# Optimization experiments

Measured on AMD Instinct MI355X. Metric: run time of the kernel, lower is better.

Reference implementation:

```python
import jax, jax.numpy as jnp
import numpy as np

B, S, H, NH, DH, F, L = 4, 2048, 512, 8, 64, 2048, 4
ALPHA = 1.0   # config.lag_time_scale_alpha
EPS = 1e-12   # BERT layer_norm_eps
MS_PER_MIN = 60.0 * 1000.0


def setup_inputs() -> dict:
    key = jax.random.key(0)
    ks = jax.random.split(key, 24)
    p = lambda k, shape: (jax.random.normal(k, shape, jnp.float32) * 0.02)
    inp = {
        "query_states": jax.random.normal(ks[0], (B, S, H), jnp.float32),
        "attention_mask": jnp.zeros((B, 1, 1, S), jnp.float32),
        "position_bias": jax.random.normal(ks[1], (1, NH, S, S), jnp.float32) * 0.02,
        "timestamp": jnp.sort(jax.random.randint(ks[2], (B, S), 0, 36_000_000, jnp.int32), axis=-1),
        # stacked per-layer parameters (L leading dim)
        "wq": p(ks[3], (L, H, H)), "bq": jnp.zeros((L, H), jnp.float32),
        "wk": p(ks[4], (L, H, H)), "bk": jnp.zeros((L, H), jnp.float32),
        "wv": p(ks[5], (L, H, H)), "bv": jnp.zeros((L, H), jnp.float32),
        "wo": p(ks[6], (L, H, H)), "bo": jnp.zeros((L, H), jnp.float32),
        "ln1_g": jnp.ones((L, H), jnp.float32), "ln1_b": jnp.zeros((L, H), jnp.float32),
        "wi": p(ks[7], (L, H, F)), "bi": jnp.zeros((L, F), jnp.float32),
        "wo2": p(ks[8], (L, F, H)), "bo2": jnp.zeros((L, H), jnp.float32),
        "ln2_g": jnp.ones((L, H), jnp.float32), "ln2_b": jnp.zeros((L, H), jnp.float32),
    }
    return inp


def _ln(x, g, b):
    m = x.mean(-1, keepdims=True)
    v = ((x - m) ** 2).mean(-1, keepdims=True)
    return (x - m) / jnp.sqrt(v + EPS) * g + b


def reference(query_states, attention_mask, position_bias, timestamp,
              wq, bq, wk, bk, wv, bv, wo, bo, ln1_g, ln1_b,
              wi, bi, wo2, bo2, ln2_g, ln2_b):
    # encoder (is_decoder=False) lag-time scale: (B,1,S,S)
    lag = (timestamp[:, None, :, None] - timestamp[:, None, None, :]).astype(jnp.float32) / MS_PER_MIN
    scale = np.sqrt(DH).astype(np.float32) - ALPHA / (jnp.clip(lag, 0.0) + 1.0) + ALPHA

    x = query_states
    for l in range(L):
        def proj(w, b):
            return (x @ w + b).reshape(B, S, NH, DH).transpose(0, 2, 1, 3)  # (B,NH,S,DH)
        q, k, v = proj(wq[l], bq[l]), proj(wk[l], bk[l]), proj(wv[l], bv[l])
        scores = jnp.einsum('bhqd,bhkd->bhqk', q, k) / scale + position_bias + attention_mask
        probs = jax.nn.softmax(scores, axis=-1)
        ctx = jnp.einsum('bhqk,bhkd->bhqd', probs, v).transpose(0, 2, 1, 3).reshape(B, S, H)
        attn = _ln(ctx @ wo[l] + bo[l] + x, ln1_g[l], ln1_b[l])
        ffn = jax.nn.gelu(attn @ wi[l] + bi[l], approximate=False) @ wo2[l] + bo2[l]
        x = _ln(ffn + attn, ln2_g[l], ln2_b[l])
    return x
```

## Files before the change

### kernel.cpp

```cpp
#include <hip/hip_runtime.h>
#include <stdint.h>

typedef unsigned short u16;
using half8   = __attribute__((ext_vector_type(8))) _Float16;
using half4v  = __attribute__((ext_vector_type(4))) _Float16;
using half2v  = __attribute__((ext_vector_type(2))) _Float16;
using float4v = __attribute__((ext_vector_type(4))) float;

#define L2E 1.4426950408889634f

__device__ inline float4v f4zero() { float4v z = {0.f, 0.f, 0.f, 0.f}; return z; }

__device__ inline u16 f2h(float f) {
  union { _Float16 h; u16 u; } v; v.h = (_Float16)f; return v.u;
}
__device__ inline float h2f(u16 u) {
  union { u16 u; _Float16 h; } v; v.u = u; return (float)v.h;
}

__device__ inline half2v cvtpk(float a, float b) {
  return __builtin_bit_cast(half2v, __builtin_amdgcn_cvt_pkrtz(a, b));
}
__device__ inline _Float16 hexp2_(_Float16 x) {
  _Float16 r;
  asm("v_exp_f16 %0, %1" : "=v"(r) : "v"(x));
  return r;
}
__device__ inline float fdot2f(half2v a, float c) {
#if __has_builtin(__builtin_amdgcn_fdot2)
  typedef __attribute__((ext_vector_type(2))) __fp16 h2r;
  return __builtin_amdgcn_fdot2(__builtin_bit_cast(h2r, a),
                                __builtin_bit_cast(h2r, 0x3C003C00u), c, false);
#else
  return c + (float)a.x + (float)a.y;
#endif
}

__device__ inline void glds16(const u16* g, u16* lds_base, int lane) {
#if __has_builtin(__builtin_amdgcn_global_load_lds)
  (void)lane;
  __builtin_amdgcn_global_load_lds((const __attribute__((address_space(1))) void*)g,
                                   (__attribute__((address_space(3))) void*)lds_base,
                                   16, 0, 0);
#else
  *(uint4*)(lds_base + (size_t)lane * 8) = *(const uint4*)g;
#endif
}

__global__ __launch_bounds__(256) void transpose_cast_kernel(
    const float* __restrict__ in, u16* __restrict__ out, int K, int N, size_t out_ls) {
  __shared__ float tile[32][33];
  const int tx = threadIdx.x & 31, ty = threadIdx.x >> 5;
  in  += (size_t)blockIdx.z * K * N;
  out += (size_t)blockIdx.z * out_ls;
  const int n  = blockIdx.x * 32 + tx;
  const int k0 = blockIdx.y * 32;
#pragma unroll
  for (int j = 0; j < 32; j += 8)
    tile[ty + j][tx] = in[(size_t)(k0 + ty + j) * N + n];
  __syncthreads();
  const int k = k0 + tx;
  const int n0 = blockIdx.x * 32;
#pragma unroll
  for (int j = 0; j < 32; j += 8)
    out[(size_t)(n0 + ty + j) * K + k] = f2h(tile[tx][ty + j]);
}

__global__ __launch_bounds__(256) void cast_kernel(const float* __restrict__ in,
                                                   u16* __restrict__ out) {
  const int i = (blockIdx.x * 256 + threadIdx.x) * 4;
  float4 t = *(const float4*)(in + i);
  ushort4 o;
  o.x = f2h(t.x); o.y = f2h(t.y); o.z = f2h(t.z); o.w = f2h(t.w);
  *(ushort4*)(out + i) = o;
}

__global__ __launch_bounds__(256) void pb_tile_kernel(const float* __restrict__ pb,
                                                      u16* __restrict__ pbT) {
  const int g  = blockIdx.x * 256 + threadIdx.x;
  const int mm = g & 15;
  const int q  = (g >> 4) & 2047;
  const int kbh = g >> 15;
  const int kb = kbh & 31, h = kbh >> 5;
  const float* src = pb + ((size_t)h * 2048 + q) * 2048 + kb * 64 + mm;
  ushort4 o;
  o.x = f2h(src[0]  * L2E);
  o.y = f2h(src[16] * L2E);
  o.z = f2h(src[32] * L2E);
  o.w = f2h(src[48] * L2E);
  *(ushort4*)(pbT + ((size_t)(h * 32 + kb) * 2048 + q) * 64 + mm * 4) = o;
}

__global__ __launch_bounds__(256) void inv_tile_kernel(const int* __restrict__ ts,
                                                       u16* __restrict__ invT) {
  const int g  = blockIdx.x * 256 + threadIdx.x;
  const int mm = g & 15;
  const int q  = (g >> 4) & 2047;
  const int kb = (g >> 15) & 31;
  const int b  = g >> 20;
  const int tq = ts[b * 2048 + q];
  ushort4 o;
  u16* op = (u16*)&o;
#pragma unroll
  for (int nb = 0; nb < 4; nb++) {
    const int k = kb * 64 + nb * 16 + mm;
    const int du = tq - ts[b * 2048 + k];
    const float u = (du > 0) ? (float)du : 0.f;
    op[nb] = f2h(fmaf(u, L2E, 86561.70245333781f) *
                 __builtin_amdgcn_rcpf(fmaf(u, 9.f, 480000.f)));
  }
  *(ushort4*)(invT + ((size_t)(b * 32 + kb) * 2048 + q) * 64 + mm * 4) = o;
}

__global__ __launch_bounds__(256) void maskts_kernel(const float* __restrict__ mask,
                                                     const int* __restrict__ ts,
                                                     float* __restrict__ maskE,
                                                     float* __restrict__ tsf) {
  const int i = blockIdx.x * 256 + threadIdx.x;
  maskE[i] = mask[i] * L2E;
  tsf[i]   = (float)ts[i];
}

template <int BM, int BN, int NN, int KK, int EPI>
__global__ __launch_bounds__(256) void gemm_kernel(
    const u16* __restrict__ A, const u16* __restrict__ Wt,
    const float* __restrict__ b0, const float* __restrict__ b1, const float* __restrict__ b2,
    const u16* __restrict__ resid,
    void* __restrict__ o0, void* __restrict__ o1, void* __restrict__ o2) {
  constexpr int FI = BM / 32;
  constexpr int FJB = BN / 32;
  constexpr int FIW = BM / 32;
  constexpr int FJW = BN / 32;
  __shared__ __align__(16) u16 As[BM * 64];
  __shared__ __align__(16) u16 Bs[BN * 64];
  const int tid = threadIdx.x, lane = tid & 63, wv = tid >> 6;
  const int quad = lane >> 4, mm = lane & 15;
  const int m0 = blockIdx.x * BM, n0 = blockIdx.y * BN;
  const int wm = (wv >> 1) * (BM / 2), wn = (wv & 1) * (BN / 2);
  const int srow = tid >> 3, slot = tid & 7;
  const int chunk = slot ^ (srow & 7);
  const u16* Ag = A  + (size_t)(m0 + srow) * KK + chunk * 8;
  const u16* Bg = Wt + (size_t)(n0 + srow) * KK + chunk * 8;
  u16* AsW = As + (size_t)(wv * 8) * 64;
  u16* BsW = Bs + (size_t)(wv * 8) * 64;
  const int sw = mm & 7;

  float4v acc[FIW][FJW];
#pragma unroll
  for (int i = 0; i < FIW; i++)
#pragma unroll
    for (int j = 0; j < FJW; j++) acc[i][j] = f4zero();

  for (int kt = 0; kt < KK; kt += 64) {
#pragma unroll
    for (int i = 0; i < FI; i++)
      glds16(Ag + (size_t)i * 32 * KK + kt, AsW + i * 32 * 64, lane);
#pragma unroll
    for (int j = 0; j < FJB; j++)
      glds16(Bg + (size_t)j * 32 * KK + kt, BsW + j * 32 * 64, lane);
    __syncthreads();
#pragma unroll
    for (int ks = 0; ks < 2; ks++) {
      half8 a[FIW], b[FJW];
#pragma unroll
      for (int i = 0; i < FIW; i++)
        a[i] = *(const half8*)(As + (size_t)(wm + i * 16 + mm) * 64 + (size_t)((ks * 4 + quad) ^ sw) * 8);
#pragma unroll
      for (int j = 0; j < FJW; j++)
        b[j] = *(const half8*)(Bs + (size_t)(wn + j * 16 + mm) * 64 + (size_t)((ks * 4 + quad) ^ sw) * 8);
#pragma unroll
      for (int i = 0; i < FIW; i++)
#pragma unroll
        for (int j = 0; j < FJW; j++)
          acc[i][j] = __builtin_amdgcn_mfma_f32_16x16x32_f16(a[i], b[j], acc[i][j], 0, 0, 0);
    }
    __syncthreads();
  }

#pragma unroll
  for (int j = 0; j < FJW; j++) {
    const int gn = n0 + wn + j * 16 + mm;
    if (EPI == 4) {
      const int which = gn >> 9, col = gn & 511, h = (gn >> 6) & 7, d = gn & 63;
      const float* bp = (which == 0) ? b0 : (which == 1) ? b1 : b2;
      const float bias = bp[col];
      u16* dst = (which == 0) ? (u16*)o0 : (which == 1) ? (u16*)o1 : (u16*)o2;
#pragma unroll
      for (int i = 0; i < FIW; i++)
#pragma unroll
        for (int r = 0; r < 4; r++) {
          const int gm = m0 + wm + i * 16 + quad * 4 + r;
          const int b_ = gm >> 11, s_ = gm & 2047;
          const float val = acc[i][j][r] + bias;
          if (which < 2)
            dst[((size_t)((b_ * 8 + h) * 2048 + s_)) * 64 + d] = f2h(val);
          else
            dst[((size_t)((b_ * 8 + h) * 64 + d)) * 2048 +
                (s_ & ~63) + (((s_ & 15) << 2) | ((s_ >> 4) & 3))] = f2h(val);
        }
    } else {
      const float bias = b0[gn];
#pragma unroll
      for (int i = 0; i < FIW; i++)
#pragma unroll
        for (int r = 0; r < 4; r++) {
          const int gm = m0 + wm + i * 16 + quad * 4 + r;
          const float val = acc[i][j][r] + bias;
          const size_t idx = (size_t)gm * NN + gn;
          if (EPI == 2) {
            ((float*)o0)[idx] = val + h2f(resid[idx]);
          } else {
            const float z  = val * 0.70710678118654752f;
            const float az = fabsf(z);
            const float t  = __builtin_amdgcn_rcpf(1.0f + 0.3275911f * az);
            const float poly = t * (0.254829592f + t * (-0.284496736f +
                               t * (1.421413741f + t * (-1.453152027f + t * 1.061405429f))));
            const float e = __builtin_amdgcn_exp2f(-az * az * L2E);
            float erf_ = 1.0f - poly * e;
            erf_ = (z < 0.0f) ? -erf_ : erf_;
            ((u16*)o0)[idx] = f2h(val * 0.5f * (1.0f + erf_));
          }
        }
    }
  }
}

template <int TILED>
__global__ __launch_bounds__(512) void flash4_kernel(
    const u16* __restrict__ Q, const u16* __restrict__ Kb, const u16* __restrict__ Vt,
    const u16* __restrict__ pbT, const u16* __restrict__ invT,
    const float* __restrict__ pb32,
    const float* __restrict__ maskE, const float* __restrict__ tsf,
    u16* __restrict__ ctx) {
  __shared__ __align__(16) u16 Kls[2][64 * 64];
  __shared__ __align__(16) u16 Vls[2][64 * 64];
  __shared__ __align__(16) u16 P[8][16 * 64];
  const int tid = threadIdx.x, lane = tid & 63, w = tid >> 6;
  const int quad = lane >> 4, mm = lane & 15;
  const int bh = blockIdx.y, b_ = bh >> 3, h_ = bh & 7;
  const int q0 = blockIdx.x * 128 + w * 16;
  const size_t qk_base = (size_t)bh * 2048 * 64;
  const size_t v_base  = (size_t)bh * 64 * 2048;
  const int srow = lane >> 3, slot = lane & 7;
  const int chunk = slot ^ srow;
  const int sw = mm & 7;

  const u16* Kgl = Kb + qk_base + (size_t)(w * 8 + srow) * 64 + chunk * 8;
  const u16* Vgl = Vt + v_base + (size_t)(w * 8 + srow) * 2048 + chunk * 8;

  glds16(Kgl, &Kls[0][(w * 8) * 64], lane);
  glds16(Vgl, &Vls[0][(w * 8) * 64], lane);

  half8 aq[2];
#pragma unroll
  for (int t = 0; t < 2; t++)
    aq[t] = *(const half8*)(Q + qk_base + (size_t)(q0 + mm) * 64 + t * 32 + quad * 8);

  float tqf[4];
  if (TILED < 2) {
#pragma unroll
    for (int r = 0; r < 4; r++) tqf[r] = tsf[b_ * 2048 + q0 + quad * 4 + r];
  }

  float l_r[4] = {0.f, 0.f, 0.f, 0.f};
  float4v o[4];
#pragma unroll
  for (int ob = 0; ob < 4; ob++) o[ob] = f4zero();

  ushort4 pbc[4], invc[4]; float tkc[4], mkc[4];
  if (TILED >= 1) {
#pragma unroll
    for (int r = 0; r < 4; r++)
      pbc[r] = *(const ushort4*)(pbT + ((size_t)(h_ * 32) * 2048 + q0 + quad * 4 + r) * 64 + mm * 4);
  }
  if (TILED == 2) {
#pragma unroll
    for (int r = 0; r < 4; r++)
      invc[r] = *(const ushort4*)(invT + ((size_t)(b_ * 32) * 2048 + q0 + quad * 4 + r) * 64 + mm * 4);
  } else {
#pragma unroll
    for (int nb = 0; nb < 4; nb++) tkc[nb] = tsf[b_ * 2048 + nb * 16 + mm];
  }
#pragma unroll
  for (int nb = 0; nb < 4; nb++) mkc[nb] = maskE[b_ * 2048 + nb * 16 + mm];

  int cur = 0;
  for (int kt = 0; kt < 32; kt++) {
    const int k0 = kt * 64;
    __syncthreads();

    const int kn = (kt < 31) ? kt + 1 : kt;
    ushort4 pbn[4], invn[4]; float tkn[4], mkn[4];
    if (TILED >= 1) {
#pragma unroll
      for (int r = 0; r < 4; r++)
        pbn[r] = *(const ushort4*)(pbT + ((size_t)(h_ * 32 + kn) * 2048 + q0 + quad * 4 + r) * 64 + mm * 4);
    }
    if (TILED == 2) {
#pragma unroll
      for (int r = 0; r < 4; r++)
        invn[r] = *(const ushort4*)(invT + ((size_t)(b_ * 32 + kn) * 2048 + q0 + quad * 4 + r) * 64 + mm * 4);
    } else {
#pragma unroll
      for (int nb = 0; nb < 4; nb++) tkn[nb] = tsf[b_ * 2048 + kn * 64 + nb * 16 + mm];
    }
#pragma unroll
    for (int nb = 0; nb < 4; nb++) mkn[nb] = maskE[b_ * 2048 + kn * 64 + nb * 16 + mm];

    if (kt < 31) {
      const size_t ko = (size_t)(kt + 1) * 4096;
      const size_t vo = (size_t)(kt + 1) * 64;
      glds16(Kgl + ko, &Kls[cur ^ 1][(w * 8) * 64], lane);
      glds16(Vgl + vo, &Vls[cur ^ 1][(w * 8) * 64], lane);
    }

    const u16* Kc = Kls[cur];
    float4v s[4];
    __builtin_amdgcn_s_setprio(1);
#pragma unroll
    for (int nb = 0; nb < 4; nb++) {
      const half8 kf0 = *(const half8*)(Kc + (size_t)(nb * 16 + mm) * 64 + (size_t)(quad ^ sw) * 8);
      const half8 kf1 = *(const half8*)(Kc + (size_t)(nb * 16 + mm) * 64 + (size_t)((4 + quad) ^ sw) * 8);
      s[nb] = __builtin_amdgcn_mfma_f32_16x16x32_f16(aq[0], kf0, f4zero(), 0, 0, 0);
      s[nb] = __builtin_amdgcn_mfma_f32_16x16x32_f16(aq[1], kf1, s[nb], 0, 0, 0);
    }
    __builtin_amdgcn_s_setprio(0);

    const half2v mk01 = cvtpk(mkc[0], mkc[1]);
    const half2v mk23 = cvtpk(mkc[2], mkc[3]);
#pragma unroll
    for (int r = 0; r < 4; r++) {
      half2v pb01, pb23, iv01, iv23;
      if (TILED >= 1) {
        pb01 = *(const half2v*)&pbc[r].x;
        pb23 = *(const half2v*)&pbc[r].z;
      } else {
        float pv[4];
#pragma unroll
        for (int nb = 0; nb < 4; nb++)
          pv[nb] = pb32[((size_t)h_ * 2048 + q0 + quad * 4 + r) * 2048 + k0 + nb * 16 + mm] * L2E;
        pb01 = cvtpk(pv[0], pv[1]); pb23 = cvtpk(pv[2], pv[3]);
      }
      if (TILED == 2) {
        iv01 = *(const half2v*)&invc[r].x;
        iv23 = *(const half2v*)&invc[r].z;
      } else {
        float ivv[4];
#pragma unroll
        for (int nb = 0; nb < 4; nb++) {
          const float u = fmaxf(tqf[r] - tkc[nb], 0.f);
          ivv[nb] = fmaf(u, L2E, 86561.70245333781f) *
                    __builtin_amdgcn_rcpf(fmaf(u, 9.f, 480000.f));
        }
        iv01 = cvtpk(ivv[0], ivv[1]); iv23 = cvtpk(ivv[2], ivv[3]);
      }
      const half2v s01 = cvtpk(s[0][r], s[1][r]);
      const half2v s23 = cvtpk(s[2][r], s[3][r]);
      const half2v t01 = __builtin_elementwise_fma(s01, iv01, pb01 + mk01);
      const half2v t23 = __builtin_elementwise_fma(s23, iv23, pb23 + mk23);
      half2v p01, p23;
      p01.x = hexp2_(t01.x); p01.y = hexp2_(t01.y);
      p23.x = hexp2_(t23.x); p23.y = hexp2_(t23.y);
      l_r[r] = fdot2f(p01, l_r[r]);
      l_r[r] = fdot2f(p23, l_r[r]);
      const int prow = quad * 4 + r;
      union { half2v h2[2]; half4v h4; } uu;
      uu.h2[0] = p01; uu.h2[1] = p23;
      *(half4v*)((char*)P[w] + prow * 128 + ((mm * 8) ^ ((prow & 7) << 4))) = uu.h4;
    }

    const u16* Vc = Vls[cur];
    const char* Pb = (const char*)P[w] + mm * 128;
    const int pxor = (mm & 7) << 4;
    const half8 ap0 = *(const half8*)(Pb + ((quad * 16) ^ pxor));
    const half8 ap1 = *(const half8*)(Pb + ((64 + quad * 16) ^ pxor));
    __builtin_amdgcn_s_setprio(1);
#pragma unroll
    for (int ob = 0; ob < 4; ob++) {
      const half8 vf0 = *(const half8*)(Vc + (size_t)(ob * 16 + mm) * 64 + (size_t)(quad ^ sw) * 8);
      const half8 vf1 = *(const half8*)(Vc + (size_t)(ob * 16 + mm) * 64 + (size_t)((4 + quad) ^ sw) * 8);
      o[ob] = __builtin_amdgcn_mfma_f32_16x16x32_f16(ap0, vf0, o[ob], 0, 0, 0);
      o[ob] = __builtin_amdgcn_mfma_f32_16x16x32_f16(ap1, vf1, o[ob], 0, 0, 0);
    }
    __builtin_amdgcn_s_setprio(0);

#pragma unroll
    for (int r = 0; r < 4; r++) { pbc[r] = pbn[r]; invc[r] = invn[r]; }
#pragma unroll
    for (int nb = 0; nb < 4; nb++) { tkc[nb] = tkn[nb]; mkc[nb] = mkn[nb]; }
    cur ^= 1;
  }

#pragma unroll
  for (int r = 0; r < 4; r++) {
    float l = l_r[r];
#pragma unroll
    for (int sh = 1; sh < 16; sh <<= 1) l += __shfl_xor(l, sh, 64);
    const float rl = __builtin_amdgcn_rcpf(l);
    const int qrow = q0 + quad * 4 + r;
#pragma unroll
    for (int ob = 0; ob < 4; ob++)
      ctx[((size_t)b_ * 2048 + qrow) * 512 + h_ * 64 + ob * 16 + mm] = f2h(o[ob][r] * rl);
  }
}

__global__ __launch_bounds__(256) void ln_kernel(
    const float* __restrict__ in, const float* __restrict__ g, const float* __restrict__ bb,
    float* __restrict__ of, u16* __restrict__ obf) {
  const int lane = threadIdx.x & 63, w = threadIdx.x >> 6;
  const int row = blockIdx.x * 4 + w;
  const float* x = in + (size_t)row * 512;
  float v[8];
  const float4 t0 = *(const float4*)(x + lane * 8);
  const float4 t1 = *(const float4*)(x + lane * 8 + 4);
  v[0] = t0.x; v[1] = t0.y; v[2] = t0.z; v[3] = t0.w;
  v[4] = t1.x; v[5] = t1.y; v[6] = t1.z; v[7] = t1.w;
  float s = 0.f;
#pragma unroll
  for (int i = 0; i < 8; i++) s += v[i];
#pragma unroll
  for (int sh = 1; sh < 64; sh <<= 1) s += __shfl_xor(s, sh, 64);
  const float mean = s * (1.0f / 512.0f);
  float sq = 0.f;
#pragma unroll
  for (int i = 0; i < 8; i++) { const float d = v[i] - mean; sq += d * d; }
#pragma unroll
  for (int sh = 1; sh < 64; sh <<= 1) sq += __shfl_xor(sq, sh, 64);
  const float rstd = rsqrtf(sq * (1.0f / 512.0f) + 1e-12f);
#pragma unroll
  for (int i = 0; i < 8; i++) {
    const int col = lane * 8 + i;
    const float y = (v[i] - mean) * rstd * g[col] + bb[col];
    if (of) of[(size_t)row * 512 + col] = y;
    obf[(size_t)row * 512 + col] = f2h(y);
  }
}

extern "C" void kernel_launch(void* const* d_in, const int* in_sizes, int n_in,
                              void* d_out, int out_size, void* d_ws, size_t ws_size,
                              hipStream_t stream) {
  const float* x_in = (const float*)d_in[0];
  const float* mask = (const float*)d_in[1];
  const float* pb   = (const float*)d_in[2];
  const int*   ts   = (const int*)d_in[3];
  const float* wq = (const float*)d_in[4];  const float* bq = (const float*)d_in[5];
  const float* wk = (const float*)d_in[6];  const float* bk = (const float*)d_in[7];
  const float* wvp = (const float*)d_in[8]; const float* bv = (const float*)d_in[9];
  const float* wo = (const float*)d_in[10]; const float* bo = (const float*)d_in[11];
  const float* ln1g = (const float*)d_in[12]; const float* ln1b = (const float*)d_in[13];
  const float* wi = (const float*)d_in[14]; const float* bi = (const float*)d_in[15];
  const float* wo2 = (const float*)d_in[16]; const float* bo2 = (const float*)d_in[17];
  const float* ln2g = (const float*)d_in[18]; const float* ln2b = (const float*)d_in[19];

  char* ws = (char*)d_ws;
  const size_t o_wqkv  = 0;
  const size_t o_woT   = 6291456;
  const size_t o_wiT   = 8388608;
  const size_t o_wo2T  = 16777216;
  const size_t o_maskE = 25165824;
  const size_t o_tsf   = 25198592;
  const size_t o_xbf   = 25231360;
  const size_t o_qb    = 33619968;
  const size_t o_kb    = 42008576;
  const size_t o_vb    = 50397184;
  const size_t o_ctx   = 58785792;
  const size_t o_attnb = 67174400;
  const size_t o_tmp   = 75563008;
  const size_t o_pbT   = 92340224;
  const size_t o_invT  = 159449088;
  const int tiled = (ws_size >= o_invT + 33554432ull) ? 2
                  : (ws_size >= o_pbT + 67108864ull) ? 1 : 0;

  u16*   wqkvT = (u16*)(ws + o_wqkv);
  u16*   woT   = (u16*)(ws + o_woT);
  u16*   wiT   = (u16*)(ws + o_wiT);
  u16*   wo2T  = (u16*)(ws + o_wo2T);
  float* maskE = (float*)(ws + o_maskE);
  float* tsf   = (float*)(ws + o_tsf);
  u16*   xbf   = (u16*)(ws + o_xbf);
  u16*   qb    = (u16*)(ws + o_qb);
  u16*   kb    = (u16*)(ws + o_kb);
  u16*   vb    = (u16*)(ws + o_vb);
  u16*   ctx   = (u16*)(ws + o_ctx);
  u16*   hb    = (u16*)(ws + o_qb);
  u16*   attnb = (u16*)(ws + o_attnb);
  float* tmp   = (float*)(ws + o_tmp);
  u16*   pbT   = (u16*)(ws + o_pbT);
  u16*   invT  = (u16*)(ws + o_invT);

  const dim3 blk(256);
  const dim3 blk512(512);
  transpose_cast_kernel<<<dim3(16, 16, 4), blk, 0, stream>>>(wq,  wqkvT,          512, 512, 786432);
  transpose_cast_kernel<<<dim3(16, 16, 4), blk, 0, stream>>>(wk,  wqkvT + 262144, 512, 512, 786432);
  transpose_cast_kernel<<<dim3(16, 16, 4), blk, 0, stream>>>(wvp, wqkvT + 524288, 512, 512, 786432);
  transpose_cast_kernel<<<dim3(16, 16, 4), blk, 0, stream>>>(wo,  woT,  512, 512,  262144);
  transpose_cast_kernel<<<dim3(64, 16, 4), blk, 0, stream>>>(wi,  wiT,  512, 2048, 1048576);
  transpose_cast_kernel<<<dim3(16, 64, 4), blk, 0, stream>>>(wo2, wo2T, 2048, 512, 1048576);
  maskts_kernel<<<32, blk, 0, stream>>>(mask, ts, maskE, tsf);
  cast_kernel<<<4096, blk, 0, stream>>>(x_in, xbf);
  if (tiled >= 1) pb_tile_kernel<<<32768, blk, 0, stream>>>(pb, pbT);
  if (tiled == 2) inv_tile_kernel<<<16384, blk, 0, stream>>>(ts, invT);

  for (int l = 0; l < 4; l++) {
    gemm_kernel<128, 128, 1536, 512, 4><<<dim3(64, 12), blk, 0, stream>>>(
        xbf, wqkvT + (size_t)l * 786432, bq + l * 512, bk + l * 512, bv + l * 512,
        nullptr, qb, kb, vb);
    if (tiled == 2)
      flash4_kernel<2><<<dim3(16, 32), blk512, 0, stream>>>(qb, kb, vb, pbT, invT, pb, maskE, tsf, ctx);
    else if (tiled == 1)
      flash4_kernel<1><<<dim3(16, 32), blk512, 0, stream>>>(qb, kb, vb, pbT, nullptr, pb, maskE, tsf, ctx);
    else
      flash4_kernel<0><<<dim3(16, 32), blk512, 0, stream>>>(qb, kb, vb, nullptr, nullptr, pb, maskE, tsf, ctx);
    gemm_kernel<128, 64, 512, 512, 2><<<dim3(64, 8), blk, 0, stream>>>(
        ctx, woT + (size_t)l * 262144, bo + l * 512, nullptr, nullptr, xbf,
        tmp, nullptr, nullptr);
    ln_kernel<<<2048, blk, 0, stream>>>(tmp, ln1g + l * 512, ln1b + l * 512, nullptr, attnb);
    gemm_kernel<128, 128, 2048, 512, 3><<<dim3(64, 16), blk, 0, stream>>>(
        attnb, wiT + (size_t)l * 1048576, bi + l * 2048, nullptr, nullptr, nullptr,
        hb, nullptr, nullptr);
    gemm_kernel<128, 64, 512, 2048, 2><<<dim3(64, 8), blk, 0, stream>>>(
        hb, wo2T + (size_t)l * 1048576, bo2 + l * 512, nullptr, nullptr, attnb,
        tmp, nullptr, nullptr);
    ln_kernel<<<2048, blk, 0, stream>>>(tmp, ln2g + l * 512, ln2b + l * 512,
                                        (l == 3) ? (float*)d_out : nullptr, xbf);
  }
  (void)in_sizes; (void)n_in; (void)out_size;
}
```

Before: 1.253 ms.

## Double-buffer GEMM shared-memory tiles to overlap global loads with MFMA

The GEMM kernel now keeps two shared-memory buffers for the A and B tiles. It prefetches the next K-tile with direct global-to-LDS loads while the current tile is fed to MFMA, and drops one of the two barriers per iteration. The aim is to hide global load latency behind compute. The cost is twice the LDS per block, which may lower occupancy. The attention loop also gets an unroll-2 hint.

```diff
diff --git a/kernel.cpp b/kernel.cpp
--- a/kernel.cpp
+++ b/kernel.cpp
@@ -131,8 +131,9 @@
   constexpr int FJB = BN / 32;
   constexpr int FIW = BM / 32;
   constexpr int FJW = BN / 32;
-  __shared__ __align__(16) u16 As[BM * 64];
-  __shared__ __align__(16) u16 Bs[BN * 64];
+  constexpr int NT = KK / 64;
+  __shared__ __align__(16) u16 As[2][BM * 64];
+  __shared__ __align__(16) u16 Bs[2][BN * 64];
   const int tid = threadIdx.x, lane = tid & 63, wv = tid >> 6;
   const int quad = lane >> 4, mm = lane & 15;
   const int m0 = blockIdx.x * BM, n0 = blockIdx.y * BN;
@@ -141,8 +142,6 @@
   const int chunk = slot ^ (srow & 7);
   const u16* Ag = A  + (size_t)(m0 + srow) * KK + chunk * 8;
   const u16* Bg = Wt + (size_t)(n0 + srow) * KK + chunk * 8;
-  u16* AsW = As + (size_t)(wv * 8) * 64;
-  u16* BsW = Bs + (size_t)(wv * 8) * 64;
   const int sw = mm & 7;
 
   float4v acc[FIW][FJW];
@@ -151,30 +150,44 @@
 #pragma unroll
     for (int j = 0; j < FJW; j++) acc[i][j] = f4zero();
 
-  for (int kt = 0; kt < KK; kt += 64) {
-#pragma unroll
-    for (int i = 0; i < FI; i++)
-      glds16(Ag + (size_t)i * 32 * KK + kt, AsW + i * 32 * 64, lane);
-#pragma unroll
-    for (int j = 0; j < FJB; j++)
-      glds16(Bg + (size_t)j * 32 * KK + kt, BsW + j * 32 * 64, lane);
+#pragma unroll
+  for (int i = 0; i < FI; i++)
+    glds16(Ag + (size_t)i * 32 * KK, &As[0][(size_t)(wv * 8 + i * 32) * 64], lane);
+#pragma unroll
+  for (int j = 0; j < FJB; j++)
+    glds16(Bg + (size_t)j * 32 * KK, &Bs[0][(size_t)(wv * 8 + j * 32) * 64], lane);
+
+  int cur = 0;
+#pragma unroll 2
+  for (int kt = 0; kt < NT; kt++) {
     __syncthreads();
+
+    if (kt + 1 < NT) {
+      const size_t ko = (size_t)(kt + 1) * 64;
+#pragma unroll
+      for (int i = 0; i < FI; i++)
+        glds16(Ag + (size_t)i * 32 * KK + ko, &As[cur ^ 1][(size_t)(wv * 8 + i * 32) * 64], lane);
+#pragma unroll
+      for (int j = 0; j < FJB; j++)
+        glds16(Bg + (size_t)j * 32 * KK + ko, &Bs[cur ^ 1][(size_t)(wv * 8 + j * 32) * 64], lane);
+    }
+
 #pragma unroll
     for (int ks = 0; ks < 2; ks++) {
       half8 a[FIW], b[FJW];
 #pragma unroll
       for (int i = 0; i < FIW; i++)
-        a[i] = *(const half8*)(As + (size_t)(wm + i * 16 + mm) * 64 + (size_t)((ks * 4 + quad) ^ sw) * 8);
+        a[i] = *(const half8*)(&As[cur][0] + (size_t)(wm + i * 16 + mm) * 64 + (size_t)((ks * 4 + quad) ^ sw) * 8);
 #pragma unroll
       for (int j = 0; j < FJW; j++)
-        b[j] = *(const half8*)(Bs + (size_t)(wn + j * 16 + mm) * 64 + (size_t)((ks * 4 + quad) ^ sw) * 8);
+        b[j] = *(const half8*)(&Bs[cur][0] + (size_t)(wn + j * 16 + mm) * 64 + (size_t)((ks * 4 + quad) ^ sw) * 8);
 #pragma unroll
       for (int i = 0; i < FIW; i++)
 #pragma unroll
         for (int j = 0; j < FJW; j++)
           acc[i][j] = __builtin_amdgcn_mfma_f32_16x16x32_f16(a[i], b[j], acc[i][j], 0, 0, 0);
     }
-    __syncthreads();
+    cur ^= 1;
   }
 
 #pragma unroll
@@ -285,6 +298,7 @@
   for (int nb = 0; nb < 4; nb++) mkc[nb] = maskE[b_ * 2048 + nb * 16 + mm];
 
   int cur = 0;
+#pragma unroll 2
   for (int kt = 0; kt < 32; kt++) {
     const int k0 = kt * 64;
     __syncthreads();
```

Result: slower. 1.392 ms (+11.1%).
